# Kernel tuning notes

Measured on AMD Instinct MI355X. Metric: run time of the kernel, lower is better.

## Reference

```python
import jax, jax.numpy as jnp
import numpy as np

B, HW, NL = 32, 1024, 64
VD, LD, H = 1024, 768, 8
EPS = 1e-5


def _bn(x, g, b):
    # x: [B, L, C]; BatchNorm1d (train mode, batch stats) over (B, L) per channel
    m = x.mean(axis=(0, 1), keepdims=True)
    v = x.var(axis=(0, 1), keepdims=True)
    return (x - m) * jax.lax.rsqrt(v + EPS) * g + b


def _inorm(x):
    # x: [B, L, C]; InstanceNorm1d (no affine): normalize over L per (sample, channel)
    m = x.mean(axis=1, keepdims=True)
    v = x.var(axis=1, keepdims=True)
    return (x - m) * jax.lax.rsqrt(v + EPS)


def _sdpa(q_in, k_in, v_in, qw, qb, kw, kb, vw, vb, ow, ob, query_mask=None, key_mask=None):
    b, nq, d = q_in.shape
    nk = k_in.shape[1]
    dk = d // H
    q = (q_in @ qw.T + qb).reshape(b, nq, H, dk).transpose(0, 2, 1, 3)  # [b,h,nq,dk]
    k = (k_in @ kw.T + kb).reshape(b, nk, H, dk).transpose(0, 2, 1, 3)  # [b,h,nk,dk]
    v = (v_in @ vw.T + vb).reshape(b, nk, H, dk).transpose(0, 2, 1, 3)  # [b,h,nk,dk]
    if query_mask is not None:
        q = q * query_mask.reshape(b, 1, nq, 1)
    if key_mask is not None:
        k = k * key_mask.reshape(b, 1, nk, 1)
        v = v * key_mask.reshape(b, 1, nk, 1)
    att = jnp.einsum('bhqd,bhkd->bhqk', q, k) / (dk ** 0.5)
    att = jax.nn.softmax(att, axis=-1)
    out = jnp.einsum('bhqk,bhkd->bhqd', att, v)
    out = out.transpose(0, 2, 1, 3).reshape(b, nq, d)
    return out @ ow.T + ob, att


def setup_inputs() -> dict:
    key = jax.random.key(0)
    ks = iter(jax.random.split(key, 64))
    d = {
        'src': jax.random.normal(next(ks), (B, HW, VD), jnp.float32),
        'lan': jax.random.normal(next(ks), (B, NL, LD), jnp.float32),
        'pos_embed': jax.random.normal(next(ks), (B, HW, VD), jnp.float32),
        'lan_attmask': jnp.ones((B, NL), jnp.float32),
        'ip_w': jax.random.normal(next(ks), (VD, VD), jnp.float32) * 0.02,
        'ip_b': jnp.zeros((VD,), jnp.float32),
        'ip_g': jnp.ones((VD,), jnp.float32),
        'ip_beta': jnp.zeros((VD,), jnp.float32),
        'lp_w': jax.random.normal(next(ks), (VD, LD), jnp.float32) * 0.02,
        'lp_b': jnp.zeros((VD,), jnp.float32),
        'mem_tok': jax.random.normal(next(ks), (1, VD), jnp.float32) * 0.02,
        'neg_mem_tok': jax.random.normal(next(ks), (1, VD), jnp.float32) * 0.02,
    }
    for pre in ('vl', 'mf', 'ff'):
        for nm in ('q', 'k', 'v', 'o'):
            d[f'{pre}_{nm}w'] = jax.random.normal(next(ks), (VD, VD), jnp.float32) * 0.02
            d[f'{pre}_{nm}b'] = jnp.zeros((VD,), jnp.float32)
    d['op_w'] = jax.random.normal(next(ks), (VD, VD), jnp.float32) * 0.02
    d['op_b'] = jnp.zeros((VD,), jnp.float32)
    d['op_g'] = jnp.ones((VD,), jnp.float32)
    d['op_beta'] = jnp.zeros((VD,), jnp.float32)
    return d


def reference(src, lan, pos_embed, lan_attmask, ip_w, ip_b, ip_g, ip_beta, lp_w, lp_b,
              mem_tok, neg_mem_tok,
              vl_qw, vl_qb, vl_kw, vl_kb, vl_vw, vl_vb, vl_ow, vl_ob,
              mf_qw, mf_qb, mf_kw, mf_kb, mf_vw, mf_vb, mf_ow, mf_ob,
              ff_qw, ff_qb, ff_kw, ff_kb, ff_vw, ff_vb, ff_ow, ff_ob,
              op_w, op_b, op_g, op_beta):
    # input/lan projections (Conv1d k=1 == per-token linear), BN on vision path
    src_p = _bn(src @ ip_w.T + ip_b, ip_g, ip_beta)          # [B,HW,VD]
    lan_p = lan @ lp_w.T + lp_b                              # [B,NL,VD]

    # stage 1: vision-language fuse (query = language, multiplicative query mask)
    vl_out, vl_att = _sdpa(lan_p, src_p, src_p,
                           vl_qw, vl_qb, vl_kw, vl_kb, vl_vw, vl_vb, vl_ow, vl_ob,
                           query_mask=lan_attmask)
    # norms[0](vl_out) is computed in the original but its result is never used downstream

    # stage 2: memory fuse (memory tokens attend over language, key mask)
    mem_q = jnp.broadcast_to(mem_tok[None], (B, 1, VD))
    mem_out, mem_att = _sdpa(mem_q, lan_p, lan_p,
                             mf_qw, mf_qb, mf_kw, mf_kb, mf_vw, mf_vb, mf_ow, mf_ob,
                             key_mask=lan_attmask)
    neg_q = jnp.broadcast_to(neg_mem_tok[None], (B, 1, VD))
    cur = jnp.concatenate([neg_q, mem_out], axis=1)          # [B,2,VD]
    cur = _inorm(cur)                                        # norms[1], L=2>1 branch

    # stage 3: feature fuse (vision queries over memory tokens)
    ff_out, ff_att = _sdpa(src_p, cur, cur,
                           ff_qw, ff_qb, ff_kw, ff_kb, ff_vw, ff_vb, ff_ow, ff_ob)
    ff_n = _inorm(ff_out)                                    # norms[2]
    final = _bn(ff_n @ op_w.T + op_b, op_g, op_beta)         # output_proj conv + BN
    return (final, cur, vl_att, mem_att, ff_att)
```

## Files before the change

### kernel.cpp

```cpp
#include <hip/hip_runtime.h>
#include <stdint.h>

#define EPS 1e-5f
#define SCALE 0.08838834764831845f

typedef __bf16 bf16x8 __attribute__((ext_vector_type(8)));
typedef float f32x4 __attribute__((ext_vector_type(4)));
typedef unsigned short u16;
typedef unsigned int u32;
typedef u16 u16x8 __attribute__((ext_vector_type(8)));

__device__ __forceinline__ u16 f2bf(float f) {
  union { float f; u32 u; } x; x.f = f;
  u32 r = x.u + 0x7fffu + ((x.u >> 16) & 1u);
  return (u16)(r >> 16);
}
__device__ __forceinline__ float bf2f(u16 u) {
  union { u32 u; float f; } x; x.u = ((u32)u) << 16; return x.f;
}
__device__ __forceinline__ void glds16(const void* g, void* l) {
  __builtin_amdgcn_global_load_lds((__attribute__((address_space(1))) void*)g,
                                   (__attribute__((address_space(3))) void*)l,
                                   16, 0, 0);
}

struct F2B8 {
  const float* in[8];
  u16* out[8];
  int n4[8];
};
__global__ __launch_bounds__(256) void f2b_multi(F2B8 j) {
  const int seg = blockIdx.y;
  const int n4 = j.n4[seg];
  const float* __restrict__ in = j.in[seg];
  u16* __restrict__ out = j.out[seg];
  for (int i = blockIdx.x * 256 + threadIdx.x; i < n4; i += gridDim.x * 256) {
    float4 v = ((const float4*)in)[i];
    ((ushort4*)out)[i] = make_ushort4(f2bf(v.x), f2bf(v.y), f2bf(v.z), f2bf(v.w));
  }
}

struct WT2 { const float* W[2]; u16* WT[2]; };
__global__ __launch_bounds__(256)
void wtrans2(WT2 g) {
  __shared__ float tile[64][65];
  const float* __restrict__ W = g.W[blockIdx.z];
  u16* __restrict__ WT = g.WT[blockIdx.z];
  const int bx = blockIdx.x, by = blockIdx.y;
  const int r = threadIdx.x >> 2, c0 = (threadIdx.x & 3) * 16;
  const float* src = W + (size_t)(by * 64 + r) * 1024 + bx * 64 + c0;
#pragma unroll
  for (int e = 0; e < 16; e += 4) {
    float4 v = *(const float4*)(src + e);
    tile[r][c0 + e] = v.x; tile[r][c0 + e + 1] = v.y;
    tile[r][c0 + e + 2] = v.z; tile[r][c0 + e + 3] = v.w;
  }
  __syncthreads();
  u16* dst = WT + (size_t)(bx * 64 + r) * 1024 + by * 64 + c0;
#pragma unroll
  for (int e = 0; e < 16; e += 4) {
    ushort4 o = make_ushort4(f2bf(tile[c0 + e][r]), f2bf(tile[c0 + e + 1][r]),
                             f2bf(tile[c0 + e + 2][r]), f2bf(tile[c0 + e + 3][r]));
    *(ushort4*)(dst + e) = o;
  }
}

__global__ __launch_bounds__(256)
void gemm_ip(const float* __restrict__ Af, const u16* __restrict__ B,
             u16* __restrict__ Cb, float* __restrict__ ps,
             float* __restrict__ pq, int M, int N, int K) {
  __shared__ u16 sA[128 * 64];
  __shared__ u16 sB[128 * 64];
  const int nwg = (int)(gridDim.x * gridDim.y);
  const int chunk = nwg >> 3;
  int s = blockIdx.y * gridDim.x + blockIdx.x;
  int t = (s & 7) * chunk + (s >> 3);
  const int bn0 = (t & 7) * 128;
  const int bm0 = (t >> 3) * 128;
  const int tid = threadIdx.x;
  const int w = tid >> 6, l = tid & 63;
  const int wr = w >> 1, wc = w & 1;
  const int lr = l & 15, lk = l >> 4;
  const int swz = lr & 7;

  const int srow = tid >> 3;
  const int lslot = tid & 7;
  const int pslot = lslot ^ (srow & 7);
  const float* As = Af + (size_t)(bm0 + srow) * K + lslot * 8;
  const int scol = pslot << 3;
  const u16* Bb = B + (size_t)(bn0 + srow) * K + scol;
  const size_t rstride32 = (size_t)32 * K;

  f32x4 acc[4][4] = {};
  f32x4 pa0[4], pa1[4];
#pragma unroll
  for (int p = 0; p < 4; ++p) {
    const float* sp = As + (size_t)p * 32 * K;
    pa0[p] = *(const f32x4*)(sp);
    pa1[p] = *(const f32x4*)(sp + 4);
  }

  for (int k0 = 0; k0 < K; k0 += 64) {
#pragma unroll
    for (int p = 0; p < 4; ++p)
      glds16(Bb + p * rstride32 + k0, sB + p * 2048 + w * 512);
#pragma unroll
    for (int p = 0; p < 4; ++p) {
      u16x8 o;
      o[0] = f2bf(pa0[p][0]); o[1] = f2bf(pa0[p][1]);
      o[2] = f2bf(pa0[p][2]); o[3] = f2bf(pa0[p][3]);
      o[4] = f2bf(pa1[p][0]); o[5] = f2bf(pa1[p][1]);
      o[6] = f2bf(pa1[p][2]); o[7] = f2bf(pa1[p][3]);
      *(u16x8*)(sA + p * 2048 + srow * 64 + (pslot << 3)) = o;
    }
    __syncthreads();
    if (k0 + 64 < K) {
#pragma unroll
      for (int p = 0; p < 4; ++p) {
        const float* sp = As + (size_t)p * 32 * K + k0 + 64;
        pa0[p] = *(const f32x4*)(sp);
        pa1[p] = *(const f32x4*)(sp + 4);
      }
    }
#pragma unroll
    for (int ks = 0; ks < 2; ++ks) {
      const int off = (((ks << 2) + lk) ^ swz) << 3;
      bf16x8 af[4], bfr[4];
#pragma unroll
      for (int m = 0; m < 4; ++m)
        af[m] = *(const bf16x8*)(sA + (wr * 64 + m * 16 + lr) * 64 + off);
#pragma unroll
      for (int n = 0; n < 4; ++n)
        bfr[n] = *(const bf16x8*)(sB + (wc * 64 + n * 16 + lr) * 64 + off);
#pragma unroll
      for (int m = 0; m < 4; ++m)
#pragma unroll
        for (int n = 0; n < 4; ++n)
          acc[m][n] = __builtin_amdgcn_mfma_f32_16x16x32_bf16(af[m], bfr[n], acc[m][n], 0, 0, 0);
    }
    __syncthreads();
  }

#pragma unroll
  for (int m = 0; m < 4; ++m) {
    const int grow0 = bm0 + wr * 64 + m * 16 + lk * 4;
#pragma unroll
    for (int n = 0; n < 4; ++n) {
      const int gcol = bn0 + wc * 64 + n * 16 + lr;
#pragma unroll
      for (int i = 0; i < 4; ++i)
        Cb[(size_t)(grow0 + i) * N + gcol] = f2bf(acc[m][n][i]);
    }
  }

  float csum[4], csq[4];
#pragma unroll
  for (int n = 0; n < 4; ++n) {
    float s2 = 0.f, q2 = 0.f;
#pragma unroll
    for (int m = 0; m < 4; ++m)
#pragma unroll
      for (int i = 0; i < 4; ++i) {
        const float v = acc[m][n][i];
        s2 += v; q2 += v * v;
      }
    s2 += __shfl_xor(s2, 16, 64); q2 += __shfl_xor(q2, 16, 64);
    s2 += __shfl_xor(s2, 32, 64); q2 += __shfl_xor(q2, 32, 64);
    csum[n] = s2; csq[n] = q2;
  }
  float* cs = (float*)sA;
  float* cq = cs + 256;
  if (lk == 0) {
#pragma unroll
    for (int n = 0; n < 4; ++n) {
      cs[wr * 128 + wc * 64 + n * 16 + lr] = csum[n];
      cq[wr * 128 + wc * 64 + n * 16 + lr] = csq[n];
    }
  }
  __syncthreads();
  if (tid < 128) {
    const size_t o = (size_t)(bm0 >> 7) * 1024 + bn0 + tid;
    ps[o] = cs[tid] + cs[128 + tid];
    pq[o] = cq[tid] + cq[128 + tid];
  }
}

__global__ __launch_bounds__(256)
void gemm_bt(const u16* __restrict__ A, const u16* __restrict__ B,
             const float* __restrict__ bias, u16* __restrict__ Cb,
             int M, int N, int K) {
  __shared__ u16 sA[128 * 64];
  __shared__ u16 sB[128 * 64];
  const int nwg = (int)(gridDim.x * gridDim.y);
  const int chunk = nwg >> 3;
  int s = blockIdx.y * gridDim.x + blockIdx.x;
  int t = (s & 7) * chunk + (s >> 3);
  const int bn0 = (t & 7) * 128;
  const int bm0 = (t >> 3) * 128;
  const int tid = threadIdx.x;
  const int w = tid >> 6, l = tid & 63;
  const int wr = w >> 1, wc = w & 1;
  const int lr = l & 15, lk = l >> 4;
  const int swz = lr & 7;

  const int srow = tid >> 3;
  const int scol = ((tid & 7) ^ (srow & 7)) << 3;
  const u16* Ab = A + (size_t)(bm0 + srow) * K + scol;
  const u16* Bb = B + (size_t)(bn0 + srow) * K + scol;
  const size_t rstride32 = (size_t)32 * K;

  f32x4 acc[4][4] = {};

  for (int k0 = 0; k0 < K; k0 += 64) {
#pragma unroll
    for (int p = 0; p < 4; ++p) {
      glds16(Ab + p * rstride32 + k0, sA + p * 2048 + w * 512);
      glds16(Bb + p * rstride32 + k0, sB + p * 2048 + w * 512);
    }
    __syncthreads();
#pragma unroll
    for (int ks = 0; ks < 2; ++ks) {
      const int off = (((ks << 2) + lk) ^ swz) << 3;
      bf16x8 af[4], bfr[4];
#pragma unroll
      for (int m = 0; m < 4; ++m)
        af[m] = *(const bf16x8*)(sA + (wr * 64 + m * 16 + lr) * 64 + off);
#pragma unroll
      for (int n = 0; n < 4; ++n)
        bfr[n] = *(const bf16x8*)(sB + (wc * 64 + n * 16 + lr) * 64 + off);
#pragma unroll
      for (int m = 0; m < 4; ++m)
#pragma unroll
        for (int n = 0; n < 4; ++n)
          acc[m][n] = __builtin_amdgcn_mfma_f32_16x16x32_bf16(af[m], bfr[n], acc[m][n], 0, 0, 0);
    }
    __syncthreads();
  }

#pragma unroll
  for (int m = 0; m < 4; ++m) {
    const int grow0 = bm0 + wr * 64 + m * 16 + lk * 4;
#pragma unroll
    for (int n = 0; n < 4; ++n) {
      const int gcol = bn0 + wc * 64 + n * 16 + lr;
      const float bv = bias ? bias[gcol] : 0.0f;
#pragma unroll
      for (int i = 0; i < 4; ++i) {
        const float v = acc[m][n][i] + bv;
        Cb[(size_t)(grow0 + i) * N + gcol] = f2bf(v);
      }
    }
  }
}

struct G3 { const u16* B[3]; const float* bias[3]; u16* C[3]; };
__global__ __launch_bounds__(256)
void gemm_bt_z(const u16* __restrict__ A, G3 g, int M, int N, int K) {
  __shared__ u16 sA[128 * 64];
  __shared__ u16 sB[128 * 64];
  const int z = blockIdx.z;
  const u16* __restrict__ B = g.B[z];
  const float* __restrict__ bias = g.bias[z];
  u16* __restrict__ Cb = g.C[z];
  const int nwg = (int)(gridDim.x * gridDim.y);
  const int chunk = nwg >> 3;
  int s = blockIdx.y * gridDim.x + blockIdx.x;
  int t = (s & 7) * chunk + (s >> 3);
  const int bn0 = (t & 7) * 128;
  const int bm0 = (t >> 3) * 128;
  const int tid = threadIdx.x;
  const int w = tid >> 6, l = tid & 63;
  const int wr = w >> 1, wc = w & 1;
  const int lr = l & 15, lk = l >> 4;
  const int swz = lr & 7;

  const int srow = tid >> 3;
  const int scol = ((tid & 7) ^ (srow & 7)) << 3;
  const u16* Ab = A + (size_t)(bm0 + srow) * K + scol;
  const u16* Bb = B + (size_t)(bn0 + srow) * K + scol;
  const size_t rstride32 = (size_t)32 * K;

  f32x4 acc[4][4] = {};

  for (int k0 = 0; k0 < K; k0 += 64) {
#pragma unroll
    for (int p = 0; p < 4; ++p) {
      glds16(Ab + p * rstride32 + k0, sA + p * 2048 + w * 512);
      glds16(Bb + p * rstride32 + k0, sB + p * 2048 + w * 512);
    }
    __syncthreads();
#pragma unroll
    for (int ks = 0; ks < 2; ++ks) {
      const int off = (((ks << 2) + lk) ^ swz) << 3;
      bf16x8 af[4], bfr[4];
#pragma unroll
      for (int m = 0; m < 4; ++m)
        af[m] = *(const bf16x8*)(sA + (wr * 64 + m * 16 + lr) * 64 + off);
#pragma unroll
      for (int n = 0; n < 4; ++n)
        bfr[n] = *(const bf16x8*)(sB + (wc * 64 + n * 16 + lr) * 64 + off);
#pragma unroll
      for (int m = 0; m < 4; ++m)
#pragma unroll
        for (int n = 0; n < 4; ++n)
          acc[m][n] = __builtin_amdgcn_mfma_f32_16x16x32_bf16(af[m], bfr[n], acc[m][n], 0, 0, 0);
    }
    __syncthreads();
  }

#pragma unroll
  for (int m = 0; m < 4; ++m) {
    const int grow0 = bm0 + wr * 64 + m * 16 + lk * 4;
#pragma unroll
    for (int n = 0; n < 4; ++n) {
      const int gcol = bn0 + wc * 64 + n * 16 + lr;
      const float bv = bias[gcol];
#pragma unroll
      for (int i = 0; i < 4; ++i)
        Cb[(size_t)(grow0 + i) * N + gcol] = f2bf(acc[m][n][i] + bv);
    }
  }
}

__global__ __launch_bounds__(256)
void gemm_qpp(const u16* __restrict__ QV, const u16* __restrict__ WT,
              const float* __restrict__ afv, u16* __restrict__ Q2) {
  __shared__ u16 sA[128 * 64];
  __shared__ u16 sB[128 * 64];
  const int h = blockIdx.z;
  int s = blockIdx.y * 8 + blockIdx.x;
  int t = (s & 7) * 16 + (s >> 3);
  const int bn0 = (t & 7) * 128;
  const int bm0 = (t >> 3) * 128;
  const int tid = threadIdx.x;
  const int w = tid >> 6, l = tid & 63;
  const int wr = w >> 1, wc = w & 1;
  const int lr = l & 15, lk = l >> 4;
  const int swz = lr & 7;

  const int srow = tid >> 3;
  const int scol = ((tid & 7) ^ (srow & 7)) << 3;
  const u16* Ab = QV + (size_t)(bm0 + srow) * 1024 + h * 128 + scol;
  const u16* Bb = WT + (size_t)(bn0 + srow) * 1024 + h * 128 + scol;
  const size_t rstride32 = (size_t)32 * 1024;

  f32x4 acc[4][4] = {};

  for (int k0 = 0; k0 < 128; k0 += 64) {
#pragma unroll
    for (int p = 0; p < 4; ++p) {
      glds16(Ab + p * rstride32 + k0, sA + p * 2048 + w * 512);
      glds16(Bb + p * rstride32 + k0, sB + p * 2048 + w * 512);
    }
    __syncthreads();
#pragma unroll
    for (int ks = 0; ks < 2; ++ks) {
      const int off = (((ks << 2) + lk) ^ swz) << 3;
      bf16x8 af[4], bfr[4];
#pragma unroll
      for (int m = 0; m < 4; ++m)
        af[m] = *(const bf16x8*)(sA + (wr * 64 + m * 16 + lr) * 64 + off);
#pragma unroll
      for (int n = 0; n < 4; ++n)
        bfr[n] = *(const bf16x8*)(sB + (wc * 64 + n * 16 + lr) * 64 + off);
#pragma unroll
      for (int m = 0; m < 4; ++m)
#pragma unroll
        for (int n = 0; n < 4; ++n)
          acc[m][n] = __builtin_amdgcn_mfma_f32_16x16x32_bf16(af[m], bfr[n], acc[m][n], 0, 0, 0);
    }
    __syncthreads();
  }

#pragma unroll
  for (int m = 0; m < 4; ++m) {
    const int grow0 = bm0 + wr * 64 + m * 16 + lk * 4;
#pragma unroll
    for (int n = 0; n < 4; ++n) {
      const int gcol = bn0 + wc * 64 + n * 16 + lr;
      const float a = afv[gcol];
#pragma unroll
      for (int i = 0; i < 4; ++i) {
        const int gr = grow0 + i;
        const int q2row = ((gr >> 6) << 9) + h * 64 + (gr & 63);
        Q2[(size_t)q2row * 1024 + gcol] = f2bf(acc[m][n][i] * a);
      }
    }
  }
}

__global__ __launch_bounds__(256)
void cst_kernel(const u16* __restrict__ QV, const float* __restrict__ wcv,
                float* __restrict__ cstv) {
  const int row = blockIdx.x * 256 + threadIdx.x;
  const int b = row >> 9, rem = row & 511;
  const int h = rem >> 6, i = rem & 63;
  const u16* q = QV + (size_t)(b * 64 + i) * 1024 + h * 128;
  const float* wv = wcv + h * 128;
  float acc = 0.f;
  for (int d = 0; d < 128; d += 8) {
    u16x8 v = *(const u16x8*)(q + d);
#pragma unroll
    for (int e = 0; e < 8; ++e) acc += bf2f(v[e]) * wv[d + e];
  }
  cstv[row] = acc;
}

__global__ __launch_bounds__(512)
void vl_fused(const u16* __restrict__ Q2, const u16* __restrict__ Y1,
              const float* __restrict__ cstv, const float* __restrict__ qmask,
              float* __restrict__ out) {
  __shared__ u16 sB[1024 * 32];
  __shared__ u16 sA[64 * 32];
  __shared__ float redmx[64][8];
  __shared__ float redsm[64][8];
  const int blk = blockIdx.x;
  const int xcd = blk & 7;
  const int idx = blk >> 3;
  const int b = xcd + 8 * (idx >> 3);
  const int r0 = (idx & 7) * 64;
  const int tid = threadIdx.x;
  const int w = tid >> 6, l = tid & 63;
  const int lr = l & 15, lk = l >> 4;

  const int arow = tid >> 2;
  const int aslot = tid & 3;
  const u16* Asrc = Q2 + (size_t)(b * 512 + r0 + arow) * 1024 +
                    ((aslot ^ (arow & 3)) << 3);
  const int brow0 = w * 16 + (l >> 2);
  const int bslot = l & 3;
  const u16* Bsrc0 = Y1 + (size_t)b * 1048576 + (size_t)brow0 * 1024 +
                     ((bslot ^ ((l >> 2) & 3)) << 3);

  f32x4 acc[4][8] = {};

  for (int k0 = 0; k0 < 1024; k0 += 32) {
    if (tid < 256) glds16(Asrc + k0, sA + w * 512);
#pragma unroll
    for (int p = 0; p < 8; ++p)
      glds16(Bsrc0 + (size_t)p * 128 * 1024 + k0, sB + (p * 8 + w) * 512);
    __syncthreads();
    const int roff = (lk ^ (lr & 3)) << 3;
    bf16x8 af[4];
#pragma unroll
    for (int m = 0; m < 4; ++m)
      af[m] = *(const bf16x8*)(sA + (m * 16 + lr) * 32 + roff);
#pragma unroll
    for (int n = 0; n < 8; ++n) {
      bf16x8 bf_ = *(const bf16x8*)(sB + (w * 128 + n * 16 + lr) * 32 + roff);
#pragma unroll
      for (int m = 0; m < 4; ++m)
        acc[m][n] = __builtin_amdgcn_mfma_f32_16x16x32_bf16(af[m], bf_, acc[m][n], 0, 0, 0);
    }
    __syncthreads();
  }

  float cst_r[4][4], scl[4][4];
#pragma unroll
  for (int m = 0; m < 4; ++m)
#pragma unroll
    for (int i = 0; i < 4; ++i) {
      const int rem = r0 + m * 16 + lk * 4 + i;
      cst_r[m][i] = cstv[b * 512 + rem];
      scl[m][i] = qmask[b * 64 + (rem & 63)] * SCALE;
    }
#pragma unroll
  for (int m = 0; m < 4; ++m)
#pragma unroll
    for (int n = 0; n < 8; ++n)
#pragma unroll
      for (int i = 0; i < 4; ++i)
        acc[m][n][i] = (acc[m][n][i] + cst_r[m][i]) * scl[m][i];

  float mx[4][4];
#pragma unroll
  for (int m = 0; m < 4; ++m)
#pragma unroll
    for (int i = 0; i < 4; ++i) {
      float v = -3.4e38f;
#pragma unroll
      for (int n = 0; n < 8; ++n) v = fmaxf(v, acc[m][n][i]);
      for (int o = 1; o < 16; o <<= 1) v = fmaxf(v, __shfl_xor(v, o, 64));
      mx[m][i] = v;
    }
  if (lr == 0) {
#pragma unroll
    for (int m = 0; m < 4; ++m)
#pragma unroll
      for (int i = 0; i < 4; ++i)
        redmx[m * 16 + lk * 4 + i][w] = mx[m][i];
  }
  __syncthreads();
#pragma unroll
  for (int m = 0; m < 4; ++m)
#pragma unroll
    for (int i = 0; i < 4; ++i) {
      const int rl = m * 16 + lk * 4 + i;
      float v = redmx[rl][0];
#pragma unroll
      for (int ww = 1; ww < 8; ++ww) v = fmaxf(v, redmx[rl][ww]);
      mx[m][i] = v;
    }

  float sm[4][4];
#pragma unroll
  for (int m = 0; m < 4; ++m)
#pragma unroll
    for (int i = 0; i < 4; ++i) {
      float s = 0.f;
#pragma unroll
      for (int n = 0; n < 8; ++n) {
        float e = expf(acc[m][n][i] - mx[m][i]);
        acc[m][n][i] = e;
        s += e;
      }
      for (int o = 1; o < 16; o <<= 1) s += __shfl_xor(s, o, 64);
      sm[m][i] = s;
    }
  if (lr == 0) {
#pragma unroll
    for (int m = 0; m < 4; ++m)
#pragma unroll
      for (int i = 0; i < 4; ++i)
        redsm[m * 16 + lk * 4 + i][w] = sm[m][i];
  }
  __syncthreads();
#pragma unroll
  for (int m = 0; m < 4; ++m)
#pragma unroll
    for (int i = 0; i < 4; ++i) {
      const int rl = m * 16 + lk * 4 + i;
      float s = 0.f;
#pragma unroll
      for (int ww = 0; ww < 8; ++ww) s += redsm[rl][ww];
      sm[m][i] = 1.0f / s;
    }

#pragma unroll
  for (int m = 0; m < 4; ++m)
#pragma unroll
    for (int i = 0; i < 4; ++i) {
      const size_t grow = (size_t)(b * 512 + r0 + m * 16 + lk * 4 + i);
#pragma unroll
      for (int n = 0; n < 8; ++n)
        out[grow * 1024 + w * 128 + n * 16 + lr] = acc[m][n][i] * sm[m][i];
    }
}

__global__ __launch_bounds__(256)
void colstats_final(const float* __restrict__ ps, const float* __restrict__ pq,
                    float2* __restrict__ st, const float* __restrict__ g,
                    const float* __restrict__ be, float* __restrict__ afv,
                    float* __restrict__ cfv, float inv_n) {
  __shared__ float rs_[8][32], rq_[8][32];
  const int cg = threadIdx.x >> 5, cl = threadIdx.x & 31;
  const int col = blockIdx.x * 32 + cl;
  float s = 0.f, q = 0.f;
  for (int i = 0; i < 32; ++i) {
    const size_t idx = (size_t)(cg * 32 + i) * 1024 + col;
    s += ps[idx]; q += pq[idx];
  }
  rs_[cg][cl] = s; rq_[cg][cl] = q;
  __syncthreads();
  if (cg == 0) {
    for (int i = 1; i < 8; ++i) { s += rs_[i][cl]; q += rq_[i][cl]; }
    const float m = s * inv_n;
    const float v = q * inv_n - m * m;
    const float rs = rsqrtf(v + EPS);
    st[col] = make_float2(m, rs);
    if (afv) {
      const float a = rs * g[col];
      afv[col] = a;
      cfv[col] = be[col] - m * a;
    }
  }
}

__global__ __launch_bounds__(256)
void small_gemm(const float* __restrict__ A, const float* __restrict__ W,
                const float* __restrict__ bias, float* __restrict__ out,
                int N, int K) {
  __shared__ float sA[1024];
  const int m = blockIdx.y;
  const int n = blockIdx.x * 256 + threadIdx.x;
  for (int i = threadIdx.x; i < K; i += 256) sA[i] = A[(size_t)m * K + i];
  __syncthreads();
  const float4* w4 = (const float4*)(W + (size_t)n * K);
  const float4* a4 = (const float4*)sA;
  float acc = bias ? bias[n] : 0.0f;
  for (int k = 0; k < K / 4; ++k) {
    float4 wv = w4[k], av = a4[k];
    acc += av.x * wv.x + av.y * wv.y + av.z * wv.z + av.w * wv.w;
  }
  out[(size_t)m * N + n] = acc;
}

struct SG2 { const float* W[2]; const float* bias[2]; float* out[2]; };
__global__ __launch_bounds__(256)
void small_gemm2(const float* __restrict__ A, SG2 g, int N, int K) {
  __shared__ float sA[1024];
  const int z = blockIdx.z;
  const int m = blockIdx.y;
  const int n = blockIdx.x * 256 + threadIdx.x;
  for (int i = threadIdx.x; i < K; i += 256) sA[i] = A[(size_t)m * K + i];
  __syncthreads();
  const float4* w4 = (const float4*)(g.W[z] + (size_t)n * K);
  const float4* a4 = (const float4*)sA;
  float acc = g.bias[z][n];
  for (int k = 0; k < K / 4; ++k) {
    float4 wv = w4[k], av = a4[k];
    acc += av.x * wv.x + av.y * wv.y + av.z * wv.z + av.w * wv.w;
  }
  g.out[z][(size_t)m * N + n] = acc;
}

struct VG2 { const float* A[2]; const float* W[2]; const float* bias[2]; float* out[2]; };
__global__ __launch_bounds__(256)
void vec_gemm2(VG2 g) {
  __shared__ float sAv[1024];
  const int z = blockIdx.z;
  const float* __restrict__ A = g.A[z];
  const float* __restrict__ W = g.W[z];
  const int tid = threadIdx.x;
  ((float4*)sAv)[tid] = ((const float4*)A)[tid];
  __syncthreads();
  const int og = tid >> 3, t8 = tid & 7;
  const int n = blockIdx.x * 32 + og;
  const float* wr = W + (size_t)n * 1024;
  float s = 0.f;
#pragma unroll
  for (int j = 0; j < 32; ++j) {
    const int k = j * 32 + t8 * 4;
    float4 wv = *(const float4*)(wr + k);
    float4 av = *(const float4*)(sAv + k);
    s += av.x * wv.x + av.y * wv.y + av.z * wv.z + av.w * wv.w;
  }
  s += __shfl_xor(s, 1, 64);
  s += __shfl_xor(s, 2, 64);
  s += __shfl_xor(s, 4, 64);
  if (t8 == 0) g.out[z][n] = s + g.bias[z][n];
}

__global__ __launch_bounds__(256)
void mem_attn(const float* __restrict__ qmf, const u16* __restrict__ KM,
              const u16* __restrict__ VM, const float* __restrict__ mask,
              float* __restrict__ att_out, float* __restrict__ attv_out) {
  __shared__ float qs[1024];
  __shared__ float sS[512];
  __shared__ float sP[512];
  __shared__ float sM[64];
  const int b = blockIdx.x;
  const int tid = threadIdx.x;
  for (int i = tid; i < 1024; i += 256) qs[i] = qmf[i];
  if (tid < 64) sM[tid] = mask[b * 64 + tid];
  __syncthreads();
  for (int p = tid; p < 512; p += 256) {
    const int h = p >> 6, j = p & 63;
    const u16* kr = KM + (size_t)(b * 64 + j) * 1024 + h * 128;
    float acc = 0.f;
    for (int d = 0; d < 128; ++d) acc += qs[h * 128 + d] * bf2f(kr[d]);
    sS[p] = acc * sM[j] * SCALE;
  }
  __syncthreads();
  if (tid < 8) {
    const int h = tid;
    float mx = -3.4e38f;
    for (int j = 0; j < 64; ++j) mx = fmaxf(mx, sS[h * 64 + j]);
    float sum = 0.f;
    for (int j = 0; j < 64; ++j) {
      float e = expf(sS[h * 64 + j] - mx);
      sP[h * 64 + j] = e; sum += e;
    }
    const float inv = 1.0f / sum;
    for (int j = 0; j < 64; ++j) {
      float pp = sP[h * 64 + j] * inv;
      sP[h * 64 + j] = pp;
      att_out[(size_t)(b * 8 + h) * 64 + j] = pp;
    }
  }
  __syncthreads();
  for (int c = tid; c < 1024; c += 256) {
    const int h = c >> 7;
    float acc = 0.f;
    for (int j = 0; j < 64; ++j)
      acc += sP[h * 64 + j] * sM[j] * bf2f(VM[(size_t)(b * 64 + j) * 1024 + c]);
    attv_out[(size_t)b * 1024 + c] = acc;
  }
}

__global__ __launch_bounds__(256)
void make_cur(const float* __restrict__ neg, const float* __restrict__ memo,
              float* __restrict__ cur_out, float* __restrict__ curw) {
  const int i = blockIdx.x * 256 + threadIdx.x;
  const int b = i >> 10, c = i & 1023;
  const float a = neg[c], x = memo[i];
  const float mean = 0.5f * (a + x);
  const float d = a - mean;
  const float rs = rsqrtf(d * d + EPS);
  const float o0 = d * rs, o1 = -d * rs;
  cur_out[(size_t)(b * 2) * 1024 + c] = o0;
  cur_out[(size_t)(b * 2 + 1) * 1024 + c] = o1;
  curw[(size_t)(b * 2) * 1024 + c] = o0;
  curw[(size_t)(b * 2 + 1) * 1024 + c] = o1;
}

__global__ __launch_bounds__(256)
void ffw_fold(const float* __restrict__ kff, const float* __restrict__ wfq,
              const float* __restrict__ qb, const float* __restrict__ afv,
              const float* __restrict__ cfv, u16* __restrict__ w2ff,
              float* __restrict__ cff) {
  __shared__ float redl[4];
  const int b = blockIdx.y, jh = blockIdx.x;
  const int j = jh >> 3, h = jh & 7;
  const int tid = threadIdx.x;
  const int m0 = tid * 4;
  const float* kp = kff + (size_t)b * 2048 + j * 1024 + h * 128;
  float a0 = 0, a1 = 0, a2 = 0, a3 = 0;
  for (int n = 0; n < 128; ++n) {
    const float kv = kp[n];
    const float4 wv = *(const float4*)(wfq + (size_t)(h * 128 + n) * 1024 + m0);
    a0 += kv * wv.x; a1 += kv * wv.y; a2 += kv * wv.z; a3 += kv * wv.w;
  }
  float cpart = a0 * cfv[m0] + a1 * cfv[m0 + 1] + a2 * cfv[m0 + 2] + a3 * cfv[m0 + 3];
  if (tid < 128) cpart += qb[h * 128 + tid] * kp[tid];
  ushort4 o = make_ushort4(f2bf(a0 * afv[m0]), f2bf(a1 * afv[m0 + 1]),
                           f2bf(a2 * afv[m0 + 2]), f2bf(a3 * afv[m0 + 3]));
  *(ushort4*)(w2ff + (size_t)(b * 16 + jh) * 1024 + m0) = o;
  for (int o2 = 32; o2 > 0; o2 >>= 1) cpart += __shfl_xor(cpart, o2, 64);
  if ((tid & 63) == 0) redl[tid >> 6] = cpart;
  __syncthreads();
  if (tid == 0) cff[b * 16 + jh] = redl[0] + redl[1] + redl[2] + redl[3];
}

__global__ __launch_bounds__(256)
void ff_score(const u16* __restrict__ Y1, const u16* __restrict__ w2ff,
              const float* __restrict__ cff, float* __restrict__ P,
              float* __restrict__ att_out) {
  __shared__ u16 sB[16 * 1024];
  const int chunk = blockIdx.x, b = blockIdx.y;
  const int tid = threadIdx.x;
  const int w = tid >> 6, l = tid & 63;
  const int lr = l & 15, lk = l >> 4;
  const int swz = lr & 7;

  {
    const int n = tid >> 4;
    const int sb = (tid & 15) * 8;
#pragma unroll
    for (int v = 0; v < 8; ++v) {
      const int sidx = sb + v;
      u16x8 val = *(const u16x8*)(w2ff + (size_t)(b * 16 + n) * 1024 + sidx * 8);
      *(u16x8*)(sB + n * 1024 + ((sidx ^ (n & 7)) << 3)) = val;
    }
  }
  __syncthreads();

  const u16* Ar = Y1 + ((size_t)(b * 1024 + chunk * 128) + w * 32 + lr) * 1024 + lk * 8;
  f32x4 acc[2] = {};
#pragma unroll 4
  for (int k0 = 0; k0 < 1024; k0 += 32) {
    bf16x8 a0 = *(const bf16x8*)(Ar + k0);
    bf16x8 a1 = *(const bf16x8*)(Ar + 16 * 1024 + k0);
    const int bs = (k0 >> 3) + lk;
    bf16x8 bf_ = *(const bf16x8*)(sB + lr * 1024 + ((bs ^ swz) << 3));
    acc[0] = __builtin_amdgcn_mfma_f32_16x16x32_bf16(a0, bf_, acc[0], 0, 0, 0);
    acc[1] = __builtin_amdgcn_mfma_f32_16x16x32_bf16(a1, bf_, acc[1], 0, 0, 0);
  }

  const float cadd = cff[b * 16 + lr];
  const int h = lr & 7, jj = lr >> 3;
#pragma unroll
  for (int m = 0; m < 2; ++m)
#pragma unroll
    for (int i = 0; i < 4; ++i) {
      const float sval = (acc[m][i] + cadd) * SCALE;
      const float other = __shfl_xor(sval, 8, 64);
      const float mx = fmaxf(sval, other);
      const float e0 = expf(sval - mx), e1 = expf(other - mx);
      const float p = e0 / (e0 + e1);
      const int trow = chunk * 128 + w * 32 + m * 16 + lk * 4 + i;
      P[((size_t)b * 1024 + trow) * 16 + lr] = p;
      att_out[((size_t)(b * 8 + h) * 1024 + trow) * 2 + jj] = p;
    }
}

__global__ __launch_bounds__(256)
void pg_kernel(const float* __restrict__ P, float* __restrict__ G,
               float* __restrict__ pbar) {
  __shared__ float Pl[128][16];
  const int b = blockIdx.x;
  const int tid = threadIdx.x;
  const int j = tid >> 4, j2 = tid & 15;
  float acc = 0.f, accp = 0.f;
  for (int c = 0; c < 8; ++c) {
    __syncthreads();
    for (int i = tid; i < 2048; i += 256)
      Pl[i >> 4][i & 15] = P[((size_t)b * 1024 + c * 128 + (i >> 4)) * 16 + (i & 15)];
    __syncthreads();
    for (int t = 0; t < 128; ++t) {
      acc += Pl[t][j] * Pl[t][j2];
      if (j == 0) accp += Pl[t][j2];
    }
  }
  G[b * 256 + tid] = acc * (1.f / 1024.f);
  if (j == 0) pbar[b * 16 + j2] = accp * (1.f / 1024.f);
}

__global__ __launch_bounds__(256)
void ufold(const float* __restrict__ vff, const u16* __restrict__ wfoT,
           float* __restrict__ U) {
  const int b = blockIdx.y, jh = blockIdx.x;
  const int j = jh >> 3, h = jh & 7;
  const int m0 = threadIdx.x * 4;
  const float* vp = vff + (size_t)b * 2048 + j * 1024 + h * 128;
  float a0 = 0, a1 = 0, a2 = 0, a3 = 0;
  for (int d = 0; d < 128; ++d) {
    const float kv = vp[d];
    ushort4 wv = *(const ushort4*)(wfoT + (size_t)(h * 128 + d) * 1024 + m0);
    a0 += kv * bf2f(wv.x); a1 += kv * bf2f(wv.y);
    a2 += kv * bf2f(wv.z); a3 += kv * bf2f(wv.w);
  }
  *(float4*)(U + (size_t)(b * 16 + jh) * 1024 + m0) = make_float4(a0, a1, a2, a3);
}

__global__ __launch_bounds__(256)
void iprep(const float* __restrict__ U, const float* __restrict__ G,
           const float* __restrict__ pbar, const float* __restrict__ ob,
           u16* __restrict__ U2b) {
  __shared__ float Gs[256], pb[16];
  const int b = blockIdx.x;
  const int tid = threadIdx.x;
  Gs[tid] = G[b * 256 + tid];
  if (tid < 16) pb[tid] = pbar[b * 16 + tid];
  __syncthreads();
  const int m0 = tid * 4;
  float rr[4], mi4[4];
#pragma unroll
  for (int e = 0; e < 4; ++e) {
    const int m = m0 + e;
    float u[16];
#pragma unroll
    for (int jj = 0; jj < 16; ++jj) u[jj] = U[(size_t)(b * 16 + jj) * 1024 + m];
    const float o = ob[m];
    float s1 = 0.f;
#pragma unroll
    for (int jj = 0; jj < 16; ++jj) s1 += pb[jj] * u[jj];
    float q = 0.f;
#pragma unroll
    for (int jj = 0; jj < 16; ++jj) {
      float gq = 0.f;
#pragma unroll
      for (int j2 = 0; j2 < 16; ++j2) gq += Gs[jj * 16 + j2] * u[j2];
      q += u[jj] * gq;
    }
    const float mean = s1 + o;
    const float e2 = q + 2.f * o * s1 + o * o;
    const float var = fmaxf(e2 - mean * mean, 0.f);
    mi4[e] = mean;
    rr[e] = rsqrtf(var + EPS);
  }
#pragma unroll
  for (int jj = 0; jj < 16; ++jj) {
    float4 u4 = *(const float4*)(U + (size_t)(b * 16 + jj) * 1024 + m0);
    ushort4 o = make_ushort4(f2bf(u4.x * rr[0]), f2bf(u4.y * rr[1]),
                             f2bf(u4.z * rr[2]), f2bf(u4.w * rr[3]));
    *(ushort4*)(U2b + (size_t)(b * 32 + jj) * 1024 + m0) = o;
  }
  float4 ob4 = *(const float4*)(ob + m0);
  ushort4 od = make_ushort4(
      f2bf((ob4.x - mi4[0]) * rr[0]), f2bf((ob4.y - mi4[1]) * rr[1]),
      f2bf((ob4.z - mi4[2]) * rr[2]), f2bf((ob4.w - mi4[3]) * rr[3]));
  *(ushort4*)(U2b + (size_t)(b * 32 + 16) * 1024 + m0) = od;
  ushort4 z = make_ushort4(0, 0, 0, 0);
#pragma unroll
  for (int jj = 17; jj < 32; ++jj)
    *(ushort4*)(U2b + (size_t)(b * 32 + jj) * 1024 + m0) = z;
}

__global__ __launch_bounds__(256)
void w2op_gemm(const u16* __restrict__ U2b, const u16* __restrict__ wop,
               float* __restrict__ W2op) {
  __shared__ u16 sA[32 * 64];
  __shared__ u16 sB[128 * 64];
  const int b = blockIdx.y;
  const int bn0 = blockIdx.x * 128;
  const int tid = threadIdx.x;
  const int w = tid >> 6, l = tid & 63;
  const int lr = l & 15, lk = l >> 4;
  const int swz = lr & 7;
  const int srow = tid >> 3;
  const int scol = ((tid & 7) ^ (srow & 7)) << 3;
  const u16* Ab = U2b + (size_t)b * 32768 + (size_t)srow * 1024 + scol;
  const u16* Bb = wop + (size_t)(bn0 + srow) * 1024 + scol;
  const size_t rstride32 = (size_t)32 * 1024;

  f32x4 acc[2][2] = {};
  for (int k0 = 0; k0 < 1024; k0 += 64) {
    glds16(Ab + k0, sA + w * 512);
#pragma unroll
    for (int p = 0; p < 4; ++p)
      glds16(Bb + p * rstride32 + k0, sB + p * 2048 + w * 512);
    __syncthreads();
#pragma unroll
    for (int ks = 0; ks < 2; ++ks) {
      const int off = (((ks << 2) + lk) ^ swz) << 3;
      bf16x8 af[2], bfr[2];
#pragma unroll
      for (int m = 0; m < 2; ++m)
        af[m] = *(const bf16x8*)(sA + (m * 16 + lr) * 64 + off);
#pragma unroll
      for (int n = 0; n < 2; ++n)
        bfr[n] = *(const bf16x8*)(sB + (w * 32 + n * 16 + lr) * 64 + off);
#pragma unroll
      for (int m = 0; m < 2; ++m)
#pragma unroll
        for (int n = 0; n < 2; ++n)
          acc[m][n] = __builtin_amdgcn_mfma_f32_16x16x32_bf16(af[m], bfr[n], acc[m][n], 0, 0, 0);
    }
    __syncthreads();
  }
#pragma unroll
  for (int m = 0; m < 2; ++m)
#pragma unroll
    for (int n = 0; n < 2; ++n)
#pragma unroll
      for (int i = 0; i < 4; ++i) {
        const int row = m * 16 + lk * 4 + i;
        const int col = bn0 + w * 32 + n * 16 + lr;
        W2op[((size_t)b * 32 + row) * 1024 + col] = acc[m][n][i];
      }
}

__global__ __launch_bounds__(256)
void znstats_part(const float* __restrict__ W2op, const float* __restrict__ G,
                  const float* __restrict__ pbar, float* __restrict__ pmu,
                  float* __restrict__ pe2) {
  __shared__ float Gs[256], pb[16];
  const int m = blockIdx.x * 256 + threadIdx.x;
  const int bg = blockIdx.y;
  float amu = 0.f, ae2 = 0.f;
  for (int bi = 0; bi < 4; ++bi) {
    const int b = bg * 4 + bi;
    __syncthreads();
    Gs[threadIdx.x] = G[b * 256 + threadIdx.x];
    if (threadIdx.x < 16) pb[threadIdx.x] = pbar[b * 16 + threadIdx.x];
    __syncthreads();
    float wv[17];
#pragma unroll
    for (int jj = 0; jj < 17; ++jj) wv[jj] = W2op[((size_t)b * 32 + jj) * 1024 + m];
    float s1 = 0.f;
#pragma unroll
    for (int jj = 0; jj < 16; ++jj) s1 += pb[jj] * wv[jj];
    float q = 0.f;
#pragma unroll
    for (int jj = 0; jj < 16; ++jj) {
      float gq = 0.f;
#pragma unroll
      for (int j2 = 0; j2 < 16; ++j2) gq += Gs[jj * 16 + j2] * wv[j2];
      q += wv[jj] * gq;
    }
    const float cz = wv[16];
    amu += s1 + cz;
    ae2 += q + 2.f * cz * s1 + cz * cz;
  }
  pmu[bg * 1024 + m] = amu;
  pe2[bg * 1024 + m] = ae2;
}

__global__ __launch_bounds__(256)
void znfin(const float* __restrict__ pmu, const float* __restrict__ pe2,
           const float* __restrict__ g, const float* __restrict__ be,
           float* __restrict__ afin, float* __restrict__ cf0) {
  const int m = blockIdx.x * 256 + threadIdx.x;
  float mu = 0.f, e2 = 0.f;
#pragma unroll
  for (int i = 0; i < 8; ++i) { mu += pmu[i * 1024 + m]; e2 += pe2[i * 1024 + m]; }
  mu *= (1.f / 32.f); e2 *= (1.f / 32.f);
  const float var = fmaxf(e2 - mu * mu, 0.f);
  const float A = rsqrtf(var + EPS) * g[m];
  afin[m] = A;
  cf0[m] = be[m] - mu * A;
}

__global__ __launch_bounds__(256)
void zfinal(const float* __restrict__ P, const float* __restrict__ W2op,
            const float* __restrict__ afin, const float* __restrict__ cf0,
            float* __restrict__ out) {
  __shared__ float PL[512];
  const int blk = blockIdx.x;
  const int b = blk >> 5;
  const int r0 = blk * 32;
  const int tid = threadIdx.x;
  const int col = tid * 4;

  f32x4 A4 = *(const f32x4*)(afin + col);
  f32x4 wreg[17];
#pragma unroll
  for (int jj = 0; jj < 17; ++jj) {
    f32x4 wv = *(const f32x4*)(W2op + ((size_t)b * 32 + jj) * 1024 + col);
    wreg[jj] = wv * A4;
  }
  const f32x4 basev = wreg[16] + *(const f32x4*)(cf0 + col);

  if (tid < 128)
    ((f32x4*)PL)[tid] = *(const f32x4*)(P + (size_t)r0 * 16 + tid * 4);
  __syncthreads();

  float* obase = out + (size_t)r0 * 1024 + col;
  for (int r = 0; r < 32; ++r) {
    const float* pr = PL + r * 16;
    f32x4 a = basev;
#pragma unroll
    for (int jj = 0; jj < 16; ++jj) a += pr[jj] * wreg[jj];
    *(f32x4*)(obase + (size_t)r * 1024) = a;
  }
}

extern "C" void kernel_launch(void* const* d_in, const int* in_sizes, int n_in,
                              void* d_out, int out_size, void* d_ws, size_t ws_size,
                              hipStream_t stream) {
  (void)in_sizes; (void)n_in; (void)out_size; (void)ws_size;

  const float* src      = (const float*)d_in[0];
  const float* lan      = (const float*)d_in[1];
  const float* qmask    = (const float*)d_in[3];
  const float* ip_w     = (const float*)d_in[4];
  const float* ip_g     = (const float*)d_in[6];
  const float* ip_beta  = (const float*)d_in[7];
  const float* lp_w     = (const float*)d_in[8];
  const float* lp_b     = (const float*)d_in[9];
  const float* mem_tok  = (const float*)d_in[10];
  const float* neg_tok  = (const float*)d_in[11];
  const float* vl_qw    = (const float*)d_in[12];
  const float* vl_qb    = (const float*)d_in[13];
  const float* vl_kw    = (const float*)d_in[14];
  const float* vl_kb    = (const float*)d_in[15];
  const float* mf_qw    = (const float*)d_in[20];
  const float* mf_qb    = (const float*)d_in[21];
  const float* mf_kw    = (const float*)d_in[22];
  const float* mf_kb    = (const float*)d_in[23];
  const float* mf_vw    = (const float*)d_in[24];
  const float* mf_vb    = (const float*)d_in[25];
  const float* mf_ow    = (const float*)d_in[26];
  const float* mf_ob    = (const float*)d_in[27];
  const float* ff_qw    = (const float*)d_in[28];
  const float* ff_qb    = (const float*)d_in[29];
  const float* ff_kw    = (const float*)d_in[30];
  const float* ff_kb    = (const float*)d_in[31];
  const float* ff_vw    = (const float*)d_in[32];
  const float* ff_vb    = (const float*)d_in[33];
  const float* ff_ow    = (const float*)d_in[34];
  const float* ff_ob    = (const float*)d_in[35];
  const float* op_w     = (const float*)d_in[36];
  const float* op_g     = (const float*)d_in[38];
  const float* op_beta  = (const float*)d_in[39];

  float* out_final = (float*)d_out;
  float* out_cur   = out_final + 33554432ull;
  float* out_vl    = out_cur + 65536ull;
  float* out_mem   = out_vl + 16777216ull;
  float* out_ff    = out_mem + 16384ull;

  char* wp = (char*)d_ws;
  auto take = [&](size_t sz) { char* r = wp; wp += (sz + 255) & ~(size_t)255; return r; };
  u16*   W1   = (u16*)  take(67108864);
  u16*   W2   = (u16*)  take(67108864);
  u16*   LP   = (u16*)  take(4194304);
  u16*   QV   = (u16*)  take(4194304);
  u16*   KM   = (u16*)  take(4194304);
  u16*   VM   = (u16*)  take(4194304);
  u16*   LANB = (u16*)  take(3145728);
  u16*   wip  = (u16*)  take(2097152);
  u16*   wlp  = (u16*)  take(1572864);
  u16*   wvq  = (u16*)  take(2097152);
  u16*   wmk  = (u16*)  take(2097152);
  u16*   wmv  = (u16*)  take(2097152);
  u16*   wop  = (u16*)  take(2097152);
  u16*   wvkT = (u16*)  take(2097152);
  u16*   wfoT = (u16*)  take(2097152);
  u16*   w2ff = (u16*)  take(1048576);
  u16*   U2b  = (u16*)  take(2097152);
  float* qmf   = (float*)take(4096);
  float* attvm = (float*)take(131072);
  float* memo  = (float*)take(131072);
  float* curw  = (float*)take(262144);
  float* kff   = (float*)take(262144);
  float* vff   = (float*)take(262144);
  float* ps    = (float*)take(1048576);
  float* pq    = (float*)take(1048576);
  float2* st1  = (float2*)take(8192);
  float* afv   = (float*)take(4096);
  float* cfv   = (float*)take(4096);
  float* wcv   = (float*)take(4096);
  float* cff   = (float*)take(2048);
  float* Pbuf  = (float*)take(2097152);
  float* Ub    = (float*)take(2097152);
  float* W2opb = (float*)take(4194304);
  float* Gb    = (float*)take(32768);
  float* pbarb = (float*)take(2048);
  float* pmu   = (float*)take(32768);
  float* pe2   = (float*)take(32768);
  float* afin  = (float*)take(4096);
  float* cf0   = (float*)take(4096);
  float* cstv  = (float*)take(65536);

  const dim3 blk(256);

  {
    F2B8 j;
    const float* ins[7] = {lan, ip_w, lp_w, vl_qw, mf_kw, mf_vw, op_w};
    u16* outs[7] = {LANB, wip, wlp, wvq, wmk, wmv, wop};
    int n4s[7] = {393216, 262144, 196608, 262144, 262144, 262144, 262144};
    for (int i = 0; i < 7; ++i) { j.in[i] = ins[i]; j.out[i] = outs[i]; j.n4[i] = n4s[i]; }
    f2b_multi<<<dim3(1024, 7), blk, 0, stream>>>(j);
  }
  {
    WT2 g;
    g.W[0] = vl_kw; g.WT[0] = wvkT;
    g.W[1] = ff_ow; g.WT[1] = wfoT;
    wtrans2<<<dim3(16, 16, 2), blk, 0, stream>>>(g);
  }

  gemm_ip<<<dim3(8, 256), blk, 0, stream>>>(src, wip, W2, ps, pq, 32768, 1024, 1024);
  colstats_final<<<dim3(32), blk, 0, stream>>>(ps, pq, st1, ip_g, ip_beta, afv, cfv, 1.0f / 32768.0f);

  gemm_bt<<<dim3(8, 16), blk, 0, stream>>>(LANB, wlp, lp_b, LP, 2048, 1024, 768);
  {
    G3 g;
    g.B[0] = wvq; g.bias[0] = vl_qb; g.C[0] = QV;
    g.B[1] = wmk; g.bias[1] = mf_kb; g.C[1] = KM;
    g.B[2] = wmv; g.bias[2] = mf_vb; g.C[2] = VM;
    gemm_bt_z<<<dim3(8, 16, 3), blk, 0, stream>>>(LP, g, 2048, 1024, 1024);
  }

  gemm_qpp<<<dim3(8, 16, 8), blk, 0, stream>>>(QV, wvkT, afv, W1);
  {
    VG2 g;
    g.A[0] = cfv;     g.W[0] = vl_kw; g.bias[0] = vl_kb; g.out[0] = wcv;
    g.A[1] = mem_tok; g.W[1] = mf_qw; g.bias[1] = mf_qb; g.out[1] = qmf;
    vec_gemm2<<<dim3(32, 1, 2), blk, 0, stream>>>(g);
  }
  cst_kernel<<<dim3(64), blk, 0, stream>>>(QV, wcv, cstv);
  vl_fused<<<dim3(256), dim3(512), 0, stream>>>(W1, W2, cstv, qmask, out_vl);

  mem_attn<<<dim3(32), blk, 0, stream>>>(qmf, KM, VM, qmask, out_mem, attvm);
  small_gemm<<<dim3(4, 32), blk, 0, stream>>>(attvm, mf_ow, mf_ob, memo, 1024, 1024);
  make_cur<<<dim3(128), blk, 0, stream>>>(neg_tok, memo, out_cur, curw);

  {
    SG2 g;
    g.W[0] = ff_kw; g.bias[0] = ff_kb; g.out[0] = kff;
    g.W[1] = ff_vw; g.bias[1] = ff_vb; g.out[1] = vff;
    small_gemm2<<<dim3(4, 64, 2), blk, 0, stream>>>(curw, g, 1024, 1024);
  }
  ffw_fold<<<dim3(16, 32), blk, 0, stream>>>(kff, ff_qw, ff_qb, afv, cfv, w2ff, cff);
  ff_score<<<dim3(8, 32), blk, 0, stream>>>(W2, w2ff, cff, Pbuf, out_ff);
  pg_kernel<<<dim3(32), blk, 0, stream>>>(Pbuf, Gb, pbarb);
  ufold<<<dim3(16, 32), blk, 0, stream>>>(vff, wfoT, Ub);
  iprep<<<dim3(32), blk, 0, stream>>>(Ub, Gb, pbarb, ff_ob, U2b);
  w2op_gemm<<<dim3(8, 32), blk, 0, stream>>>(U2b, wop, W2opb);
  znstats_part<<<dim3(4, 8), blk, 0, stream>>>(W2opb, Gb, pbarb, pmu, pe2);
  znfin<<<dim3(4), blk, 0, stream>>>(pmu, pe2, op_g, op_beta, afin, cf0);
  zfinal<<<dim3(1024), blk, 0, stream>>>(Pbuf, W2opb, afin, cf0, out_final);
}
```

Baseline: 598.7 us.

## Stream B operand directly from global in vl_fused and split pg reduction

```diff
diff --git a/kernel.cpp b/kernel.cpp
--- a/kernel.cpp
+++ b/kernel.cpp
@@ -410,8 +410,7 @@
 void vl_fused(const u16* __restrict__ Q2, const u16* __restrict__ Y1,
               const float* __restrict__ cstv, const float* __restrict__ qmask,
               float* __restrict__ out) {
-  __shared__ u16 sB[1024 * 32];
-  __shared__ u16 sA[64 * 32];
+  __shared__ u16 sA[2 * 8192];
   __shared__ float redmx[64][8];
   __shared__ float redsm[64][8];
   const int blk = blockIdx.x;
@@ -423,36 +422,46 @@
   const int w = tid >> 6, l = tid & 63;
   const int lr = l & 15, lk = l >> 4;
 
-  const int arow = tid >> 2;
-  const int aslot = tid & 3;
-  const u16* Asrc = Q2 + (size_t)(b * 512 + r0 + arow) * 1024 +
-                    ((aslot ^ (arow & 3)) << 3);
-  const int brow0 = w * 16 + (l >> 2);
-  const int bslot = l & 3;
-  const u16* Bsrc0 = Y1 + (size_t)b * 1048576 + (size_t)brow0 * 1024 +
-                     ((bslot ^ ((l >> 2) & 3)) << 3);
+  const int arow0 = tid >> 4;
+  const int aslot = tid & 15;
+  const u16* Asrc0 = Q2 + (size_t)(b * 512 + r0 + arow0) * 1024 +
+                     ((aslot ^ (arow0 & 7)) << 3);
+  const u16* Asrc1 = Q2 + (size_t)(b * 512 + r0 + 32 + arow0) * 1024 +
+                     ((aslot ^ ((32 + arow0) & 7)) << 3);
+  const u16* Brow = Y1 + (size_t)b * 1048576 + (size_t)(w * 128 + lr) * 1024 + lk * 8;
 
   f32x4 acc[4][8] = {};
 
-  for (int k0 = 0; k0 < 1024; k0 += 32) {
-    if (tid < 256) glds16(Asrc + k0, sA + w * 512);
-#pragma unroll
-    for (int p = 0; p < 8; ++p)
-      glds16(Bsrc0 + (size_t)p * 128 * 1024 + k0, sB + (p * 8 + w) * 512);
-    __syncthreads();
-    const int roff = (lk ^ (lr & 3)) << 3;
-    bf16x8 af[4];
-#pragma unroll
-    for (int m = 0; m < 4; ++m)
-      af[m] = *(const bf16x8*)(sA + (m * 16 + lr) * 32 + roff);
-#pragma unroll
-    for (int n = 0; n < 8; ++n) {
-      bf16x8 bf_ = *(const bf16x8*)(sB + (w * 128 + n * 16 + lr) * 32 + roff);
-#pragma unroll
-      for (int m = 0; m < 4; ++m)
-        acc[m][n] = __builtin_amdgcn_mfma_f32_16x16x32_bf16(af[m], bf_, acc[m][n], 0, 0, 0);
-    }
-    __syncthreads();
+  glds16(Asrc0, sA + w * 512);
+  glds16(Asrc1, sA + 4096 + w * 512);
+
+  for (int c = 0; c < 8; ++c) {
+    __syncthreads();
+    const u16* sAc = sA + (c & 1) * 8192;
+    if (c < 7) {
+      const int k1 = (c + 1) * 128;
+      u16* d = sA + ((c + 1) & 1) * 8192;
+      glds16(Asrc0 + k1, d + w * 512);
+      glds16(Asrc1 + k1, d + 4096 + w * 512);
+    }
+    const int k0 = c * 128;
+#pragma unroll
+    for (int ks = 0; ks < 4; ++ks) {
+      bf16x8 af[4];
+#pragma unroll
+      for (int m = 0; m < 4; ++m) {
+        const int row = m * 16 + lr;
+        af[m] = *(const bf16x8*)(sAc + row * 128 + ((((ks << 2) + lk) ^ (lr & 7)) << 3));
+      }
+      const int kc = k0 + (ks << 5);
+#pragma unroll
+      for (int n = 0; n < 8; ++n) {
+        bf16x8 bf_ = *(const bf16x8*)(Brow + (size_t)n * 16384 + kc);
+#pragma unroll
+        for (int m = 0; m < 4; ++m)
+          acc[m][n] = __builtin_amdgcn_mfma_f32_16x16x32_bf16(af[m], bf_, acc[m][n], 0, 0, 0);
+      }
+    }
   }
 
   float cst_r[4][4], scl[4][4];
@@ -785,25 +794,38 @@
 }
 
 __global__ __launch_bounds__(256)
-void pg_kernel(const float* __restrict__ P, float* __restrict__ G,
-               float* __restrict__ pbar) {
+void pg_part(const float* __restrict__ P, float* __restrict__ Gp,
+             float* __restrict__ pbarp) {
   __shared__ float Pl[128][16];
-  const int b = blockIdx.x;
+  const int b = blockIdx.x, c = blockIdx.y;
   const int tid = threadIdx.x;
   const int j = tid >> 4, j2 = tid & 15;
+  for (int i = tid; i < 2048; i += 256)
+    Pl[i >> 4][i & 15] = P[((size_t)b * 1024 + c * 128 + (i >> 4)) * 16 + (i & 15)];
+  __syncthreads();
   float acc = 0.f, accp = 0.f;
-  for (int c = 0; c < 8; ++c) {
-    __syncthreads();
-    for (int i = tid; i < 2048; i += 256)
-      Pl[i >> 4][i & 15] = P[((size_t)b * 1024 + c * 128 + (i >> 4)) * 16 + (i & 15)];
-    __syncthreads();
-    for (int t = 0; t < 128; ++t) {
-      acc += Pl[t][j] * Pl[t][j2];
-      if (j == 0) accp += Pl[t][j2];
-    }
-  }
-  G[b * 256 + tid] = acc * (1.f / 1024.f);
-  if (j == 0) pbar[b * 16 + j2] = accp * (1.f / 1024.f);
+  for (int t = 0; t < 128; ++t) {
+    acc += Pl[t][j] * Pl[t][j2];
+    if (j == 0) accp += Pl[t][j2];
+  }
+  Gp[(size_t)(b * 8 + c) * 256 + tid] = acc;
+  if (j == 0) pbarp[(b * 8 + c) * 16 + j2] = accp;
+}
+
+__global__ __launch_bounds__(256)
+void pg_fin(const float* __restrict__ Gp, const float* __restrict__ pbarp,
+            float* __restrict__ G, float* __restrict__ pbar) {
+  const int b = blockIdx.x, tid = threadIdx.x;
+  float s = 0.f;
+#pragma unroll
+  for (int c = 0; c < 8; ++c) s += Gp[(size_t)(b * 8 + c) * 256 + tid];
+  G[b * 256 + tid] = s * (1.f / 1024.f);
+  if (tid < 16) {
+    float p = 0.f;
+#pragma unroll
+    for (int c = 0; c < 8; ++c) p += pbarp[(b * 8 + c) * 16 + tid];
+    pbar[b * 16 + tid] = p * (1.f / 1024.f);
+  }
 }
 
 __global__ __launch_bounds__(256)
@@ -1098,6 +1120,8 @@
   float* W2opb = (float*)take(4194304);
   float* Gb    = (float*)take(32768);
   float* pbarb = (float*)take(2048);
+  float* Gpart = (float*)take(262144);
+  float* pbpart= (float*)take(16384);
   float* pmu   = (float*)take(32768);
   float* pe2   = (float*)take(32768);
   float* afin  = (float*)take(4096);
@@ -1155,7 +1179,8 @@
   }
   ffw_fold<<<dim3(16, 32), blk, 0, stream>>>(kff, ff_qw, ff_qb, afv, cfv, w2ff, cff);
   ff_score<<<dim3(8, 32), blk, 0, stream>>>(W2, w2ff, cff, Pbuf, out_ff);
-  pg_kernel<<<dim3(32), blk, 0, stream>>>(Pbuf, Gb, pbarb);
+  pg_part<<<dim3(32, 8), blk, 0, stream>>>(Pbuf, Gpart, pbpart);
+  pg_fin<<<dim3(32), blk, 0, stream>>>(Gpart, pbpart, Gb, pbarb);
   ufold<<<dim3(16, 32), blk, 0, stream>>>(vff, wfoT, Ub);
   iprep<<<dim3(32), blk, 0, stream>>>(Ub, Gb, pbarb, ff_ob, U2b);
   w2op_gemm<<<dim3(8, 32), blk, 0, stream>>>(U2b, wop, W2opb);
```

Result: no change. 599.8 us (+0.2%).
